# Optimization experiments

Measured on AMD Instinct MI355X. Metric: run time of the kernel, lower is better.

Reference implementation:

```python
import jax, jax.numpy as jnp
import numpy as np

SOBEL_X = jnp.array([[1., 0., -1.], [2., 0., -2.], [1., 0., -1.]], dtype=jnp.float32).reshape(1, 1, 3, 3)
SOBEL_Y = jnp.array([[1., 2., 1.], [0., 0., 0.], [-1., -2., -1.]], dtype=jnp.float32).reshape(1, 1, 3, 3)
EPS = 1e-3


def _sobel(img, kern):
    # img: [N, 1, H, W]; 3x3 conv, zero padding 1 (torch Conv2d padding=1)
    return jax.lax.conv_general_dilated(
        img, kern, window_strides=(1, 1), padding='SAME',
        dimension_numbers=('NCHW', 'OIHW', 'NCHW'))


def _compute_flow(frames):
    # frames: [B, T, 3, H, W] -> flow: [B, T-1, 2, H, W]
    B, T, C, H, W = frames.shape
    gray = (0.2989 * frames[:, :, 0] + 0.587 * frames[:, :, 1]
            + 0.114 * frames[:, :, 2])  # [B, T, H, W]
    I1 = gray[:, :-1].reshape(B * (T - 1), 1, H, W)
    I2 = gray[:, 1:].reshape(B * (T - 1), 1, H, W)
    Ix = _sobel(I1, SOBEL_X)
    Iy = _sobel(I1, SOBEL_Y)
    It = I2 - I1
    denom = Ix * Ix + Iy * Iy + EPS
    u = -Ix * It / denom
    v = -Iy * It / denom
    return jnp.concatenate([u, v], axis=1).reshape(B, T - 1, 2, H, W)


def setup_inputs() -> dict:
    key = jax.random.key(0)
    k1, k2 = jax.random.split(key)
    shape = (8, 8, 3, 256, 256)  # [B, T, C, H, W]
    pred = jax.random.uniform(k1, shape, dtype=jnp.float32)
    gt = jax.random.uniform(k2, shape, dtype=jnp.float32)
    return {"pred": pred, "gt": gt}


def reference(pred, gt):
    pred_flow = _compute_flow(pred)  # [B, T-1, 2, H, W]
    gt_flow = _compute_flow(gt)
    # motion magnitude: mean abs frame diff over channels, broadcast over 2 flow channels
    motion_mag = jnp.abs(gt[:, 1:] - gt[:, :-1]).mean(axis=2, keepdims=True)  # [B, T-1, 1, H, W]
    flow_loss = (jnp.abs(pred_flow - gt_flow) * motion_mag).mean()
    return flow_loss
```

## Files before the change

kernel.cpp:

```cpp
#include <hip/hip_runtime.h>

#define BB 8
#define TT 8
#define NPAIR (TT - 1)
#define HH 256
#define WW 256
#define FRAME_PIX (HH * WW)
#define XW 128
#define RROWS 8
#define NYT (HH / RROWS)
#define NXT (WW / XW)
#define PADW 136
#define NBLK (NYT * NXT * NPAIR * BB)
#define EPS 1e-3f
#define INV_N (1.0f / (float)((size_t)BB * NPAIR * 2 * HH * WW))

__device__ __forceinline__ float4 ld4(const float* __restrict__ p) {
    return *reinterpret_cast<const float4*>(p);
}
__device__ __forceinline__ void st4(float* p, const float4 v) {
    *reinterpret_cast<float4*>(p) = v;
}
__device__ __forceinline__ float4 gray4(const float4 r, const float4 g, const float4 b) {
    float4 o;
    o.x = 0.2989f * r.x + 0.587f * g.x + 0.114f * b.x;
    o.y = 0.2989f * r.y + 0.587f * g.y + 0.114f * b.y;
    o.z = 0.2989f * r.z + 0.587f * g.z + 0.114f * b.z;
    o.w = 0.2989f * r.w + 0.587f * g.w + 0.114f * b.w;
    return o;
}

__global__ __launch_bounds__(256, 6) void flow_loss_kernel(
    const float* __restrict__ pred, const float* __restrict__ gt,
    float* __restrict__ partial)
{
    __shared__ float gbuf[2][RROWS + 2][PADW];

    const int ytile = blockIdx.x >> 1;
    const int xtile = blockIdx.x & 1;
    const int t     = blockIdx.y;
    const int b     = blockIdx.z;
    const int y0    = ytile * RROWS;
    const int x0    = xtile * XW;
    const int tid   = threadIdx.x;
    const size_t fs = (size_t)3 * FRAME_PIX;
    const float* p1 = pred + (size_t)b * TT * fs + (size_t)t * fs;
    const float* g1 = gt   + (size_t)b * TT * fs + (size_t)t * fs;
    const float* p2 = p1 + fs;
    const float* g2 = g1 + fs;

    const int r  = tid >> 5;
    const int cx = (tid & 31) * 4;
    const size_t coff = (size_t)(y0 + r) * WW + (x0 + cx);

    bool e_act = false, e_val = false;
    int  e_img = 0;
    size_t e_off = 0;
    float* e_dst = &gbuf[0][0][0];
    if (tid < 128) {
        e_act = true;
        e_img = tid >> 6;
        const int rsel = (tid >> 5) & 1;
        const int ec   = (tid & 31) * 4;
        const int ey   = rsel ? (y0 + RROWS) : (y0 - 1);
        e_val = (unsigned)ey < HH;
        e_off = e_val ? ((size_t)ey * WW + x0 + ec) : 0;
        e_dst = &gbuf[e_img][rsel ? RROWS + 1 : 0][4 + ec];
    } else if (tid < 168) {
        const int j = tid - 128;
        e_act = true;
        e_img = j / 20;
        const int rem  = j % 20;
        const int side = rem / 10;
        const int prow = rem % 10;
        const int ey = y0 - 1 + prow;
        const int ex = side ? (x0 + XW) : (x0 - 4);
        e_val = ((unsigned)ey < HH) && ((unsigned)ex < WW);
        e_off = e_val ? ((size_t)ey * WW + ex) : 0;
        e_dst = &gbuf[e_img][prow][side ? 4 + XW : 0];
    }

    float4 e0 = make_float4(0.f, 0.f, 0.f, 0.f), e1 = e0, e2 = e0;
    if (e_act && e_val) {
        const float* eb = e_img ? g1 : p1;
        e0 = ld4(eb + e_off);
        e1 = ld4(eb + e_off + FRAME_PIX);
        e2 = ld4(eb + e_off + 2 * FRAME_PIX);
    }

    const float4 b1r = ld4(g1 + coff);
    const float4 b1g = ld4(g1 + coff + FRAME_PIX);
    const float4 b1b = ld4(g1 + coff + 2 * FRAME_PIX);
    const float4 b2r = ld4(g2 + coff);
    const float4 b2g = ld4(g2 + coff + FRAME_PIX);
    const float4 b2b = ld4(g2 + coff + 2 * FRAME_PIX);

    float mm[4];
    mm[0] = (fabsf(b2r.x - b1r.x) + fabsf(b2g.x - b1g.x) + fabsf(b2b.x - b1b.x)) * (1.f / 3.f);
    mm[1] = (fabsf(b2r.y - b1r.y) + fabsf(b2g.y - b1g.y) + fabsf(b2b.y - b1b.y)) * (1.f / 3.f);
    mm[2] = (fabsf(b2r.z - b1r.z) + fabsf(b2g.z - b1g.z) + fabsf(b2b.z - b1b.z)) * (1.f / 3.f);
    mm[3] = (fabsf(b2r.w - b1r.w) + fabsf(b2g.w - b1g.w) + fabsf(b2b.w - b1b.w)) * (1.f / 3.f);
    st4(&gbuf[1][r + 1][4 + cx], gray4(b1r, b1g, b1b));
    const float4 gg2 = gray4(b2r, b2g, b2b);

    const float4 a1r = ld4(p1 + coff);
    const float4 a1g = ld4(p1 + coff + FRAME_PIX);
    const float4 a1b = ld4(p1 + coff + 2 * FRAME_PIX);
    const float4 a2r = ld4(p2 + coff);
    const float4 a2g = ld4(p2 + coff + FRAME_PIX);
    const float4 a2b = ld4(p2 + coff + 2 * FRAME_PIX);
    st4(&gbuf[0][r + 1][4 + cx], gray4(a1r, a1g, a1b));
    const float4 gp2 = gray4(a2r, a2g, a2b);

    if (e_act) st4(e_dst, gray4(e0, e1, e2));

    __syncthreads();

    float s = 0.f;
    float up[4], vp[4];
    #pragma unroll
    for (int img = 0; img < 2; ++img) {
        float w0[6], w1[6], w2[6];
        {
            const float* p = &gbuf[img][r][cx];
            const float4 A = ld4(p), B = ld4(p + 4), C = ld4(p + 8);
            w0[0] = A.w; w0[1] = B.x; w0[2] = B.y; w0[3] = B.z; w0[4] = B.w; w0[5] = C.x;
        }
        {
            const float* p = &gbuf[img][r + 1][cx];
            const float4 A = ld4(p), B = ld4(p + 4), C = ld4(p + 8);
            w1[0] = A.w; w1[1] = B.x; w1[2] = B.y; w1[3] = B.z; w1[4] = B.w; w1[5] = C.x;
        }
        {
            const float* p = &gbuf[img][r + 2][cx];
            const float4 A = ld4(p), B = ld4(p + 4), C = ld4(p + 8);
            w2[0] = A.w; w2[1] = B.x; w2[2] = B.y; w2[3] = B.z; w2[4] = B.w; w2[5] = C.x;
        }
        const float4 gr2 = img ? gg2 : gp2;
        const float g2a[4] = {gr2.x, gr2.y, gr2.z, gr2.w};
        #pragma unroll
        for (int j = 0; j < 4; ++j) {
            const float Ix = (w0[j] - w0[j + 2]) + 2.0f * (w1[j] - w1[j + 2]) + (w2[j] - w2[j + 2]);
            const float Iy = (w0[j] + 2.0f * w0[j + 1] + w0[j + 2])
                           - (w2[j] + 2.0f * w2[j + 1] + w2[j + 2]);
            const float It = g2a[j] - w1[j + 1];
            const float inv = 1.0f / (Ix * Ix + Iy * Iy + EPS);
            if (img == 0) {
                up[j] = -(Ix * It) * inv;
                vp[j] = -(Iy * It) * inv;
            } else {
                s += (fabsf(up[j] + (Ix * It) * inv) + fabsf(vp[j] + (Iy * It) * inv)) * mm[j];
            }
        }
    }

    #pragma unroll
    for (int off = 32; off > 0; off >>= 1) s += __shfl_down(s, off, 64);

    __shared__ float wsum[4];
    if ((tid & 63) == 0) wsum[tid >> 6] = s;
    __syncthreads();
    if (tid == 0) {
        partial[((b * NPAIR) + t) * (NYT * NXT) + blockIdx.x] =
            wsum[0] + wsum[1] + wsum[2] + wsum[3];
    }
}

__global__ __launch_bounds__(896) void reduce_kernel(
    const float* __restrict__ partial, float* __restrict__ out)
{
    const float4 v = ld4(partial + threadIdx.x * 4);
    float s = (v.x + v.y) + (v.z + v.w);
    #pragma unroll
    for (int off = 32; off > 0; off >>= 1) s += __shfl_down(s, off, 64);

    __shared__ float wsum[14];
    if ((threadIdx.x & 63) == 0) wsum[threadIdx.x >> 6] = s;
    __syncthreads();
    if (threadIdx.x == 0) {
        float tot = 0.f;
        #pragma unroll
        for (int i = 0; i < 14; ++i) tot += wsum[i];
        out[0] = tot * INV_N;
    }
}

extern "C" void kernel_launch(void* const* d_in, const int* in_sizes, int n_in,
                              void* d_out, int out_size, void* d_ws, size_t ws_size,
                              hipStream_t stream) {
    const float* pred = (const float*)d_in[0];
    const float* gt   = (const float*)d_in[1];
    float* partial    = (float*)d_ws;
    float* out        = (float*)d_out;

    dim3 grid(NYT * NXT, NPAIR, BB);
    dim3 block(256);
    flow_loss_kernel<<<grid, block, 0, stream>>>(pred, gt, partial);
    reduce_kernel<<<1, 896, 0, stream>>>(partial, out);
}
```

Measured before the change: 120.9 us.

## Replace shared-memory tiles with per-wave row strips using shuffles for neighbors

Each 64-lane wave now processes a full-width strip of 4 rows for one (b,t) pair. It keeps a rolling 3-row window of grayscale rows in registers and gets horizontal neighbors through lane shuffles, instead of staging a halo tile in LDS behind __syncthreads. This removes the shared-memory staging, the halo-loader thread logic and the block barrier, and each wave writes its own partial sum. In exchange, the vertical halo is reloaded per 4-row strip, so more first-frame rows are read from global memory, and occupancy hints drop to 4 blocks per CU.

```diff
diff --git a/kernel.cpp b/kernel.cpp
--- a/kernel.cpp
+++ b/kernel.cpp
@@ -6,20 +6,15 @@
 #define HH 256
 #define WW 256
 #define FRAME_PIX (HH * WW)
-#define XW 128
-#define RROWS 8
-#define NYT (HH / RROWS)
-#define NXT (WW / XW)
-#define PADW 136
-#define NBLK (NYT * NXT * NPAIR * BB)
+#define RROWS 4
+#define NSTRIP (HH / RROWS)
+#define NITEM (BB * NPAIR * NSTRIP)
+#define NBLK (NITEM / 4)
 #define EPS 1e-3f
 #define INV_N (1.0f / (float)((size_t)BB * NPAIR * 2 * HH * WW))
 
 __device__ __forceinline__ float4 ld4(const float* __restrict__ p) {
     return *reinterpret_cast<const float4*>(p);
-}
-__device__ __forceinline__ void st4(float* p, const float4 v) {
-    *reinterpret_cast<float4*>(p) = v;
 }
 __device__ __forceinline__ float4 gray4(const float4 r, const float4 g, const float4 b) {
     float4 o;
@@ -30,140 +25,129 @@
     return o;
 }
 
-__global__ __launch_bounds__(256, 6) void flow_loss_kernel(
+struct GRow { float l; float4 g; float r; };
+
+__device__ __forceinline__ GRow mk_grow(const float4 gg, const int lane) {
+    GRow o;
+    o.g = gg;
+    const float lw = __shfl_up(gg.w, 1, 64);
+    const float rx = __shfl_down(gg.x, 1, 64);
+    o.l = (lane == 0) ? 0.f : lw;
+    o.r = (lane == 63) ? 0.f : rx;
+    return o;
+}
+
+__device__ __forceinline__ void win6(const GRow& a, float w[6]) {
+    w[0] = a.l; w[1] = a.g.x; w[2] = a.g.y; w[3] = a.g.z; w[4] = a.g.w; w[5] = a.r;
+}
+
+__device__ __forceinline__ void ld3(const float* __restrict__ base, const int y,
+                                    const int X, float4& c0, float4& c1, float4& c2) {
+    if ((unsigned)y < (unsigned)HH) {
+        const float* q = base + (size_t)y * WW + X;
+        c0 = ld4(q); c1 = ld4(q + FRAME_PIX); c2 = ld4(q + 2 * FRAME_PIX);
+    } else {
+        c0 = make_float4(0.f, 0.f, 0.f, 0.f); c1 = c0; c2 = c0;
+    }
+}
+
+__global__ __launch_bounds__(256, 4) void flow_loss_kernel(
     const float* __restrict__ pred, const float* __restrict__ gt,
     float* __restrict__ partial)
 {
-    __shared__ float gbuf[2][RROWS + 2][PADW];
+    const int tid   = threadIdx.x;
+    const int lane  = tid & 63;
+    const int item  = blockIdx.x * 4 + (tid >> 6);
+    const int strip = item & (NSTRIP - 1);
+    const int pbt   = item >> 6;
+    const int b     = pbt / NPAIR;
+    const int t     = pbt - b * NPAIR;
 
-    const int ytile = blockIdx.x >> 1;
-    const int xtile = blockIdx.x & 1;
-    const int t     = blockIdx.y;
-    const int b     = blockIdx.z;
-    const int y0    = ytile * RROWS;
-    const int x0    = xtile * XW;
-    const int tid   = threadIdx.x;
     const size_t fs = (size_t)3 * FRAME_PIX;
-    const float* p1 = pred + (size_t)b * TT * fs + (size_t)t * fs;
-    const float* g1 = gt   + (size_t)b * TT * fs + (size_t)t * fs;
+    const float* p1 = pred + ((size_t)b * TT + t) * fs;
+    const float* g1 = gt   + ((size_t)b * TT + t) * fs;
     const float* p2 = p1 + fs;
     const float* g2 = g1 + fs;
 
-    const int r  = tid >> 5;
-    const int cx = (tid & 31) * 4;
-    const size_t coff = (size_t)(y0 + r) * WW + (x0 + cx);
+    const int X  = lane * 4;
+    const int y0 = strip * RROWS;
 
-    bool e_act = false, e_val = false;
-    int  e_img = 0;
-    size_t e_off = 0;
-    float* e_dst = &gbuf[0][0][0];
-    if (tid < 128) {
-        e_act = true;
-        e_img = tid >> 6;
-        const int rsel = (tid >> 5) & 1;
-        const int ec   = (tid & 31) * 4;
-        const int ey   = rsel ? (y0 + RROWS) : (y0 - 1);
-        e_val = (unsigned)ey < HH;
-        e_off = e_val ? ((size_t)ey * WW + x0 + ec) : 0;
-        e_dst = &gbuf[e_img][rsel ? RROWS + 1 : 0][4 + ec];
-    } else if (tid < 168) {
-        const int j = tid - 128;
-        e_act = true;
-        e_img = j / 20;
-        const int rem  = j % 20;
-        const int side = rem / 10;
-        const int prow = rem % 10;
-        const int ey = y0 - 1 + prow;
-        const int ex = side ? (x0 + XW) : (x0 - 4);
-        e_val = ((unsigned)ey < HH) && ((unsigned)ex < WW);
-        e_off = e_val ? ((size_t)ey * WW + ex) : 0;
-        e_dst = &gbuf[e_img][prow][side ? 4 + XW : 0];
+    GRow rp[3], rg[3];
+    float4 k0, k1, k2;
+
+    {
+        float4 a0, a1, a2, c0, c1, c2;
+        ld3(p1, y0 - 1, X, a0, a1, a2);
+        ld3(g1, y0 - 1, X, c0, c1, c2);
+        rp[0] = mk_grow(gray4(a0, a1, a2), lane);
+        rg[0] = mk_grow(gray4(c0, c1, c2), lane);
+        ld3(p1, y0, X, a0, a1, a2);
+        ld3(g1, y0, X, k0, k1, k2);
+        rp[1] = mk_grow(gray4(a0, a1, a2), lane);
+        rg[1] = mk_grow(gray4(k0, k1, k2), lane);
     }
 
-    float4 e0 = make_float4(0.f, 0.f, 0.f, 0.f), e1 = e0, e2 = e0;
-    if (e_act && e_val) {
-        const float* eb = e_img ? g1 : p1;
-        e0 = ld4(eb + e_off);
-        e1 = ld4(eb + e_off + FRAME_PIX);
-        e2 = ld4(eb + e_off + 2 * FRAME_PIX);
-    }
+    float s = 0.f;
+    #pragma unroll
+    for (int k = 0; k < RROWS; ++k) {
+        const int ti = k % 3, mi = (k + 1) % 3, bi = (k + 2) % 3;
+        const int y  = y0 + k;
 
-    const float4 b1r = ld4(g1 + coff);
-    const float4 b1g = ld4(g1 + coff + FRAME_PIX);
-    const float4 b1b = ld4(g1 + coff + 2 * FRAME_PIX);
-    const float4 b2r = ld4(g2 + coff);
-    const float4 b2g = ld4(g2 + coff + FRAME_PIX);
-    const float4 b2b = ld4(g2 + coff + 2 * FRAME_PIX);
+        float4 pb0, pb1, pb2, gb0, gb1, gb2;
+        float4 pc0, pc1, pc2, gc0, gc1, gc2;
+        ld3(p1, y + 1, X, pb0, pb1, pb2);
+        ld3(g1, y + 1, X, gb0, gb1, gb2);
+        ld3(p2, y, X, pc0, pc1, pc2);
+        ld3(g2, y, X, gc0, gc1, gc2);
 
-    float mm[4];
-    mm[0] = (fabsf(b2r.x - b1r.x) + fabsf(b2g.x - b1g.x) + fabsf(b2b.x - b1b.x)) * (1.f / 3.f);
-    mm[1] = (fabsf(b2r.y - b1r.y) + fabsf(b2g.y - b1g.y) + fabsf(b2b.y - b1b.y)) * (1.f / 3.f);
-    mm[2] = (fabsf(b2r.z - b1r.z) + fabsf(b2g.z - b1g.z) + fabsf(b2b.z - b1b.z)) * (1.f / 3.f);
-    mm[3] = (fabsf(b2r.w - b1r.w) + fabsf(b2g.w - b1g.w) + fabsf(b2b.w - b1b.w)) * (1.f / 3.f);
-    st4(&gbuf[1][r + 1][4 + cx], gray4(b1r, b1g, b1b));
-    const float4 gg2 = gray4(b2r, b2g, b2b);
+        float mmA[4];
+        mmA[0] = (fabsf(gc0.x - k0.x) + fabsf(gc1.x - k1.x) + fabsf(gc2.x - k2.x)) * (1.f / 3.f);
+        mmA[1] = (fabsf(gc0.y - k0.y) + fabsf(gc1.y - k1.y) + fabsf(gc2.y - k2.y)) * (1.f / 3.f);
+        mmA[2] = (fabsf(gc0.z - k0.z) + fabsf(gc1.z - k1.z) + fabsf(gc2.z - k2.z)) * (1.f / 3.f);
+        mmA[3] = (fabsf(gc0.w - k0.w) + fabsf(gc1.w - k1.w) + fabsf(gc2.w - k2.w)) * (1.f / 3.f);
 
-    const float4 a1r = ld4(p1 + coff);
-    const float4 a1g = ld4(p1 + coff + FRAME_PIX);
-    const float4 a1b = ld4(p1 + coff + 2 * FRAME_PIX);
-    const float4 a2r = ld4(p2 + coff);
-    const float4 a2g = ld4(p2 + coff + FRAME_PIX);
-    const float4 a2b = ld4(p2 + coff + 2 * FRAME_PIX);
-    st4(&gbuf[0][r + 1][4 + cx], gray4(a1r, a1g, a1b));
-    const float4 gp2 = gray4(a2r, a2g, a2b);
+        const float4 gp2c = gray4(pc0, pc1, pc2);
+        const float4 gg2c = gray4(gc0, gc1, gc2);
 
-    if (e_act) st4(e_dst, gray4(e0, e1, e2));
+        rp[bi] = mk_grow(gray4(pb0, pb1, pb2), lane);
+        rg[bi] = mk_grow(gray4(gb0, gb1, gb2), lane);
+        k0 = gb0; k1 = gb1; k2 = gb2;
 
-    __syncthreads();
-
-    float s = 0.f;
-    float up[4], vp[4];
-    #pragma unroll
-    for (int img = 0; img < 2; ++img) {
-        float w0[6], w1[6], w2[6];
+        float up[4], vp[4];
         {
-            const float* p = &gbuf[img][r][cx];
-            const float4 A = ld4(p), B = ld4(p + 4), C = ld4(p + 8);
-            w0[0] = A.w; w0[1] = B.x; w0[2] = B.y; w0[3] = B.z; w0[4] = B.w; w0[5] = C.x;
+            float w0[6], w1[6], w2[6];
+            win6(rp[ti], w0); win6(rp[mi], w1); win6(rp[bi], w2);
+            const float gA[4] = {gp2c.x, gp2c.y, gp2c.z, gp2c.w};
+            #pragma unroll
+            for (int j = 0; j < 4; ++j) {
+                const float Ix = (w0[j] - w0[j + 2]) + 2.0f * (w1[j] - w1[j + 2]) + (w2[j] - w2[j + 2]);
+                const float Iy = (w0[j] + 2.0f * w0[j + 1] + w0[j + 2])
+                               - (w2[j] + 2.0f * w2[j + 1] + w2[j + 2]);
+                const float It = gA[j] - w1[j + 1];
+                const float inv = 1.0f / (Ix * Ix + Iy * Iy + EPS);
+                up[j] = -(Ix * It) * inv;
+                vp[j] = -(Iy * It) * inv;
+            }
         }
         {
-            const float* p = &gbuf[img][r + 1][cx];
-            const float4 A = ld4(p), B = ld4(p + 4), C = ld4(p + 8);
-            w1[0] = A.w; w1[1] = B.x; w1[2] = B.y; w1[3] = B.z; w1[4] = B.w; w1[5] = C.x;
-        }
-        {
-            const float* p = &gbuf[img][r + 2][cx];
-            const float4 A = ld4(p), B = ld4(p + 4), C = ld4(p + 8);
-            w2[0] = A.w; w2[1] = B.x; w2[2] = B.y; w2[3] = B.z; w2[4] = B.w; w2[5] = C.x;
-        }
-        const float4 gr2 = img ? gg2 : gp2;
-        const float g2a[4] = {gr2.x, gr2.y, gr2.z, gr2.w};
-        #pragma unroll
-        for (int j = 0; j < 4; ++j) {
-            const float Ix = (w0[j] - w0[j + 2]) + 2.0f * (w1[j] - w1[j + 2]) + (w2[j] - w2[j + 2]);
-            const float Iy = (w0[j] + 2.0f * w0[j + 1] + w0[j + 2])
-                           - (w2[j] + 2.0f * w2[j + 1] + w2[j + 2]);
-            const float It = g2a[j] - w1[j + 1];
-            const float inv = 1.0f / (Ix * Ix + Iy * Iy + EPS);
-            if (img == 0) {
-                up[j] = -(Ix * It) * inv;
-                vp[j] = -(Iy * It) * inv;
-            } else {
-                s += (fabsf(up[j] + (Ix * It) * inv) + fabsf(vp[j] + (Iy * It) * inv)) * mm[j];
+            float w0[6], w1[6], w2[6];
+            win6(rg[ti], w0); win6(rg[mi], w1); win6(rg[bi], w2);
+            const float gA[4] = {gg2c.x, gg2c.y, gg2c.z, gg2c.w};
+            #pragma unroll
+            for (int j = 0; j < 4; ++j) {
+                const float Ix = (w0[j] - w0[j + 2]) + 2.0f * (w1[j] - w1[j + 2]) + (w2[j] - w2[j + 2]);
+                const float Iy = (w0[j] + 2.0f * w0[j + 1] + w0[j + 2])
+                               - (w2[j] + 2.0f * w2[j + 1] + w2[j + 2]);
+                const float It = gA[j] - w1[j + 1];
+                const float inv = 1.0f / (Ix * Ix + Iy * Iy + EPS);
+                s += (fabsf(up[j] + (Ix * It) * inv) + fabsf(vp[j] + (Iy * It) * inv)) * mmA[j];
             }
         }
     }
 
     #pragma unroll
     for (int off = 32; off > 0; off >>= 1) s += __shfl_down(s, off, 64);
-
-    __shared__ float wsum[4];
-    if ((tid & 63) == 0) wsum[tid >> 6] = s;
-    __syncthreads();
-    if (tid == 0) {
-        partial[((b * NPAIR) + t) * (NYT * NXT) + blockIdx.x] =
-            wsum[0] + wsum[1] + wsum[2] + wsum[3];
-    }
+    if (lane == 0) partial[item] = s;
 }
 
 __global__ __launch_bounds__(896) void reduce_kernel(
@@ -193,8 +177,6 @@
     float* partial    = (float*)d_ws;
     float* out        = (float*)d_out;
 
-    dim3 grid(NYT * NXT, NPAIR, BB);
-    dim3 block(256);
-    flow_loss_kernel<<<grid, block, 0, stream>>>(pred, gt, partial);
+    flow_loss_kernel<<<dim3(NBLK), dim3(256), 0, stream>>>(pred, gt, partial);
     reduce_kernel<<<1, 896, 0, stream>>>(partial, out);
 }
```

Measured after the change: 173.9 us. 1.44x slower.
